# Performance work log

Measured on AMD Instinct MI355X. Metric: run time of the kernel, lower is better.

## Reference

```python
import jax, jax.numpy as jnp
import numpy as np

H = 8  # n_heads (init_kwarg, closed over)


def setup_inputs() -> dict:
    key = jax.random.key(0)
    ks = jax.random.split(key, 5)
    B, T, D, L = 8, 4096, 512, 128
    # lecun_normal: std = 1/sqrt(fan_in), fan_in = first dim here
    X = jax.random.normal(ks[0], (B, T, D), dtype=jnp.float32)
    Wk = jax.random.normal(ks[1], (D, L), dtype=jnp.float32) / np.sqrt(D)
    Wq = jax.random.normal(ks[2], (D, L), dtype=jnp.float32) / np.sqrt(D)
    Wv = jax.random.normal(ks[3], (D, D), dtype=jnp.float32) / np.sqrt(D)
    o_proj = jax.random.normal(ks[4], (D, D), dtype=jnp.float32) / np.sqrt(D)
    return {"X": X, "Wk": Wk, "Wq": Wq, "Wv": Wv, "o_proj": o_proj}


def reference(X, Wk, Wq, Wv, o_proj):
    B, T, D = X.shape
    L = Wk.shape[1]
    Dh, Lh = D // H, L // H
    # time-major projections: (T, B, H, *)
    V = jnp.einsum('DM,BTD->TBM', Wv, X).reshape(T, B, H, Dh)
    Q = jnp.einsum('DL,BTD->TBL', Wq, X).reshape(T, B, H, Lh)
    K = jnp.einsum('DL,BTD->TBL', Wk, X).reshape(T, B, H, Lh)
    scale = jax.lax.rsqrt(jnp.array(Dh, dtype=jnp.float32))
    K_exp = jnp.exp(K * scale)                      # (T,B,H,Lh)
    alpha = jnp.cumsum(K_exp, axis=0)               # causal normalizer
    Qs = jax.nn.softmax(Q * scale, axis=-1) / alpha # (T,B,H,Lh)

    def step(carry, args):
        qs_t, ke_t, v_t = args
        carry = carry + jnp.einsum('bhl,bhd->bhld', ke_t, v_t)
        y_t = jnp.einsum('bhl,bhld->bhd', qs_t, carry)
        return carry, y_t

    init = jnp.zeros((B, H, Lh, Dh), dtype=X.dtype)
    _, y = jax.lax.scan(step, init, (Qs, K_exp, V), unroll=16)  # y: (T,B,H,Dh)
    # faithful to source: transpose(3,0,1,2) then reshape(B,T,D)
    y = y.transpose(3, 0, 1, 2).reshape(B, T, D)
    return y @ o_proj
```

## Files before the change

### kernel.cpp

```cpp
#include <hip/hip_runtime.h>
#include <hip/hip_bf16.h>

#define B_ 8
#define T_ 4096
#define D_ 512
#define L_ 128
#define H_ 8
#define Dh_ 64
#define Lh_ 16
#define M_ (B_*T_)
#define SCALE 0.125f

typedef __bf16 v8bf __attribute__((ext_vector_type(8)));
typedef float  v4f  __attribute__((ext_vector_type(4)));
typedef unsigned short u16;
typedef u16 v8u __attribute__((ext_vector_type(8)));

__device__ __forceinline__ float b2f(u16 h){
    unsigned int u = ((unsigned int)h) << 16;
    return __builtin_bit_cast(float, u);
}
__device__ __forceinline__ u16 f2bf(float f){
    unsigned int u = __builtin_bit_cast(unsigned int, f);
    u += 0x7FFFu + ((u >> 16) & 1u);
    return (u16)(u >> 16);
}

__device__ __forceinline__ void wave_fence() {
    asm volatile("" ::: "memory");
}

__device__ __forceinline__ void gload16(const u16* g, u16* l) {
    __builtin_amdgcn_global_load_lds(
        (const __attribute__((address_space(1))) unsigned int*)(g),
        (__attribute__((address_space(3))) unsigned int*)(l), 16, 0, 0);
}

__global__ __launch_bounds__(256) void prep(
        const float* __restrict__ X,  const float* __restrict__ Wq,
        const float* __restrict__ Wk, const float* __restrict__ Wv,
        const float* __restrict__ Wo,
        u16* __restrict__ Xb, u16* __restrict__ WT, u16* __restrict__ OT)
{
    int bid = blockIdx.x;
    if (bid < 8192) {
        const size_t i = (size_t)bid * 256 + threadIdx.x;
        const float4* s = (const float4*)X + i * 2;
        float4 a = s[0], b = s[1];
        v8u o;
        o[0] = f2bf(a.x); o[1] = f2bf(a.y); o[2] = f2bf(a.z); o[3] = f2bf(a.w);
        o[4] = f2bf(b.x); o[5] = f2bf(b.y); o[6] = f2bf(b.z); o[7] = f2bf(b.w);
        *((v8u*)Xb + i) = o;
        return;
    }
    bid -= 8192;
    const float* src; u16* dst; int cols, bx, by;
    if (bid < 64)       { src = Wq; dst = WT;             cols = 128; bx = bid & 3;  by = bid >> 2; }
    else if (bid < 128) { src = Wk; dst = WT + 128 * 512; cols = 128; bid -= 64;  bx = bid & 3;  by = bid >> 2; }
    else if (bid < 384) { src = Wv; dst = WT + 256 * 512; cols = 512; bid -= 128; bx = bid & 15; by = bid >> 4; }
    else                { src = Wo; dst = OT;             cols = 512; bid -= 384; bx = bid & 15; by = bid >> 4; }
    __shared__ u16 tile[32][33];
    const int tx = threadIdx.x & 31, ty = threadIdx.x >> 5;
    const int c0 = bx * 32, r0 = by * 32;
    #pragma unroll
    for (int i = 0; i < 32; i += 8)
        tile[ty + i][tx] = f2bf(src[(size_t)(r0 + ty + i) * cols + c0 + tx]);
    __syncthreads();
    #pragma unroll
    for (int i = 0; i < 32; i += 8)
        dst[(size_t)(c0 + ty + i) * 512 + r0 + tx] = tile[tx][ty + i];
}

template<int MODE, int NY>
__global__ __launch_bounds__(256) void gemm_mfma(
        const u16* __restrict__ A, const u16* __restrict__ Bt,
        float* __restrict__ Qo, u16* __restrict__ KEo,
        u16* __restrict__ Vo, float* __restrict__ OutF)
{
    __shared__ __align__(16) u16 As[128 * 64];
    __shared__ __align__(16) u16 Bs[128 * 64];
    const int tid  = threadIdx.x;
    const int wave = tid >> 6, lane = tid & 63;
    const int wm = wave >> 1, wn = wave & 1;
    const int lm = lane & 15, quad = lane >> 4;

    const int bid = blockIdx.x;
    const int xcd = bid & 7, j = bid >> 3;
    const int grp = j / (8 * NY), r = j % (8 * NY);
    const int by  = r >> 3, pin = r & 7;
    const int bx  = xcd * 32 + grp * 8 + pin;
    const int gm0 = bx * 128, gn0 = by * 128;

    const int srow0 = wave * 32 + (lane >> 3);
    const int sg    = lane & 7;

    v4f acc[4][4];
    #pragma unroll
    for (int i = 0; i < 4; i++)
        #pragma unroll
        for (int j2 = 0; j2 < 4; j2++)
            acc[i][j2] = (v4f){0.f, 0.f, 0.f, 0.f};

    for (int kt = 0; kt < 8; ++kt) {
        const int k0 = kt * 64;
        #pragma unroll
        for (int rr = 0; rr < 4; ++rr) {
            const int row = srow0 + rr * 8;
            const int col = ((sg ^ (row & 7)) << 3) + k0;
            gload16(&A [(size_t)(gm0 + row) * 512 + col], &As[(wave * 4 + rr) * 512]);
            gload16(&Bt[(size_t)(gn0 + row) * 512 + col], &Bs[(wave * 4 + rr) * 512]);
        }
        __syncthreads();
        v8bf af[2][4], bfr[2][4];
        #pragma unroll
        for (int ks = 0; ks < 2; ks++)
            #pragma unroll
            for (int mi = 0; mi < 4; mi++) {
                const int g  = ks * 4 + quad;
                const int ra = wm * 64 + mi * 16 + lm;
                const int rb = wn * 64 + mi * 16 + lm;
                af [ks][mi] = *(const v8bf*)&As[ra * 64 + ((g ^ (ra & 7)) << 3)];
                bfr[ks][mi] = *(const v8bf*)&Bs[rb * 64 + ((g ^ (rb & 7)) << 3)];
            }
        #pragma unroll
        for (int ks = 0; ks < 2; ks++)
            #pragma unroll
            for (int mi = 0; mi < 4; mi++)
                #pragma unroll
                for (int ni = 0; ni < 4; ni++)
                    acc[mi][ni] = __builtin_amdgcn_mfma_f32_16x16x32_bf16(
                                      af[ks][mi], bfr[ks][ni], acc[mi][ni], 0, 0, 0);
        __syncthreads();
    }

    if (MODE == 1) {
        #pragma unroll
        for (int mi = 0; mi < 4; mi++)
          #pragma unroll
          for (int ni = 0; ni < 4; ni++)
            #pragma unroll
            for (int i = 0; i < 4; i++) {
                int row = gm0 + wm * 64 + mi * 16 + quad * 4 + i;
                int col = gn0 + wn * 64 + ni * 16 + lm;
                OutF[(size_t)row * 512 + col] = acc[mi][ni][i];
            }
    } else if (gn0 == 0) {
        #pragma unroll
        for (int mi = 0; mi < 4; mi++)
          #pragma unroll
          for (int ni = 0; ni < 4; ni++)
            #pragma unroll
            for (int i = 0; i < 4; i++) {
                int row = gm0 + wm * 64 + mi * 16 + quad * 4 + i;
                int col = wn * 64 + ni * 16 + lm;
                float qv = acc[mi][ni][i] * SCALE;
                float m = qv;
                #pragma unroll
                for (int off = 1; off < 16; off <<= 1) m = fmaxf(m, __shfl_xor(m, off));
                float e = __expf(qv - m);
                float s = e;
                #pragma unroll
                for (int off = 1; off < 16; off <<= 1) s += __shfl_xor(s, off);
                Qo[(size_t)row * 128 + col] = e / s;
            }
    } else if (gn0 == 128) {
        #pragma unroll
        for (int mi = 0; mi < 4; mi++)
          #pragma unroll
          for (int ni = 0; ni < 4; ni++)
            #pragma unroll
            for (int i = 0; i < 4; i++) {
                int row = gm0 + wm * 64 + mi * 16 + quad * 4 + i;
                int col = wn * 64 + ni * 16 + lm;
                KEo[(size_t)row * 128 + col] = f2bf(__expf(acc[mi][ni][i] * SCALE));
            }
    } else {
        #pragma unroll
        for (int mi = 0; mi < 4; mi++)
          #pragma unroll
          for (int ni = 0; ni < 4; ni++)
            #pragma unroll
            for (int i = 0; i < 4; i++) {
                int row = gm0 + wm * 64 + mi * 16 + quad * 4 + i;
                int col = gn0 + wn * 64 + ni * 16 + lm - 256;
                Vo[(size_t)row * 512 + col] = f2bf(acc[mi][ni][i]);
            }
    }
}

__global__ __launch_bounds__(256, 2) void chunk_sums_mfma(
        const u16* __restrict__ KE, const u16* __restrict__ V,
        float* __restrict__ Mc, float* __restrict__ AB)
{
    struct CLDS { u16 KA[16][72]; u16 VT[64][72]; };
    __shared__ __align__(16) CLDS lds[4];
    const int tid = threadIdx.x, wave = tid >> 6, lane = tid & 63;
    const int lm = lane & 15, quad = lane >> 4;
    const int ch = blockIdx.x * 4 + wave;
    const int bh = ch >> 6, c = ch & 63, b = bh >> 3, h = bh & 7;
    const int t0 = b * T_ + c * 64;
    CLDS& L = lds[wave];

    {
        const u16* kp = KE + (size_t)(t0 + lane) * L_ + h * Lh_;
        v8u k0 = *(const v8u*)kp, k1 = *(const v8u*)(kp + 8);
        #pragma unroll
        for (int l = 0; l < 8; l++) L.KA[l][lane]     = k0[l];
        #pragma unroll
        for (int l = 0; l < 8; l++) L.KA[l + 8][lane] = k1[l];
        const u16* vp = V + (size_t)(t0 + lane) * D_ + h * Dh_;
        #pragma unroll
        for (int seg = 0; seg < 8; ++seg) {
            v8u pv = *(const v8u*)(vp + seg * 8);
            #pragma unroll
            for (int j = 0; j < 8; j++) L.VT[seg * 8 + j][lane] = pv[j];
        }
    }
    wave_fence();

    v8bf ka[2];
    #pragma unroll
    for (int ki = 0; ki < 2; ki++)
        ka[ki] = *(const v8bf*)&L.KA[lm][ki * 32 + quad * 8];

    v8u onesu;
    #pragma unroll
    for (int j = 0; j < 8; j++) onesu[j] = 0x3F80;
    v8bf ones = __builtin_bit_cast(v8bf, onesu);

    v4f accL = (v4f){0.f, 0.f, 0.f, 0.f};
    accL = __builtin_amdgcn_mfma_f32_16x16x32_bf16(ka[0], ones, accL, 0, 0, 0);
    accL = __builtin_amdgcn_mfma_f32_16x16x32_bf16(ka[1], ones, accL, 0, 0, 0);

    v4f accM[4];
    #pragma unroll
    for (int nd = 0; nd < 4; nd++) accM[nd] = (v4f){0.f, 0.f, 0.f, 0.f};
    #pragma unroll
    for (int nd = 0; nd < 4; nd++)
        #pragma unroll
        for (int ki = 0; ki < 2; ki++) {
            v8bf vb = *(const v8bf*)&L.VT[nd * 16 + lm][ki * 32 + quad * 8];
            accM[nd] = __builtin_amdgcn_mfma_f32_16x16x32_bf16(ka[ki], vb, accM[nd], 0, 0, 0);
        }

    float* mcb = Mc + (size_t)ch * 1024;
    #pragma unroll
    for (int nd = 0; nd < 4; nd++)
        #pragma unroll
        for (int i = 0; i < 4; i++)
            mcb[(quad * 4 + i) * 64 + nd * 16 + lm] = accM[nd][i];
    if (lm == 0) {
        #pragma unroll
        for (int i = 0; i < 4; i++) AB[ch * 16 + quad * 4 + i] = accL[i];
    }
}

__global__ __launch_bounds__(256) void chunk_prefix(
        const float* __restrict__ Mc, u16* __restrict__ McB,
        float* __restrict__ AB)
{
    const int bh = blockIdx.x >> 2, qq = blockIdx.x & 3;
    const int i = qq * 256 + threadIdx.x;
    const size_t base = (size_t)bh * 64 * 1024 + i;
    float v[64];
    #pragma unroll
    for (int c = 0; c < 64; ++c) v[c] = Mc[base + (size_t)c * 1024];
    float run = 0.f;
    #pragma unroll
    for (int c = 0; c < 64; ++c) {
        McB[base + (size_t)c * 1024] = f2bf(run);
        run += v[c];
    }
    if (qq == 0 && threadIdx.x < 16) {
        const int l = threadIdx.x;
        float a[64];
        #pragma unroll
        for (int c = 0; c < 64; ++c) a[c] = AB[(bh * 64 + c) * 16 + l];
        float r2 = 0.f;
        #pragma unroll
        for (int c = 0; c < 64; ++c) {
            AB[(bh * 64 + c) * 16 + l] = r2;
            r2 += a[c];
        }
    }
}

__global__ __launch_bounds__(256, 2) void intra_mfma(
        const float* __restrict__ QS, const u16* __restrict__ KE,
        const u16* __restrict__ V, const u16* __restrict__ McB,
        const float* __restrict__ AB, u16* __restrict__ Y)
{
    struct ILDS {
        union {
            struct { u16 KA[16][72]; u16 Sc[16][72]; u16 qs[64][40]; } s;
            u16 p[64][72];
        } r;
        u16 VT[64][72];
    };
    __shared__ __align__(16) ILDS lds[4];
    const int tid = threadIdx.x, wave = tid >> 6, lane = tid & 63;
    const int lm = lane & 15, quad = lane >> 4;
    const int ch = blockIdx.x * 4 + wave;
    const int bh = ch >> 6, c = ch & 63, b = bh >> 3, h = bh & 7;
    const int t0 = b * T_ + c * 64;
    ILDS& L = lds[wave];

    {
        const u16* kp = KE + (size_t)(t0 + lane) * L_ + h * Lh_;
        v8u k0 = *(const v8u*)kp, k1 = *(const v8u*)(kp + 8);
        #pragma unroll
        for (int l = 0; l < 8; l++) L.r.s.KA[l][lane]     = k0[l];
        #pragma unroll
        for (int l = 0; l < 8; l++) L.r.s.KA[l + 8][lane] = k1[l];
        const u16* vp = V + (size_t)(t0 + lane) * D_ + h * Dh_;
        #pragma unroll
        for (int seg = 0; seg < 8; ++seg) {
            v8u pv = *(const v8u*)(vp + seg * 8);
            #pragma unroll
            for (int j = 0; j < 8; j++) L.VT[seg * 8 + j][lane] = pv[j];
        }
        const u16* mcb = McB + (size_t)ch * 1024;
        #pragma unroll
        for (int l = 0; l < 16; l++)
            L.r.s.Sc[l][lane] = mcb[l * 64 + lane];
        v8u z8;
        #pragma unroll
        for (int j = 0; j < 8; j++) z8[j] = 0;
        *(v8u*)&L.r.s.qs[lane][16] = z8;
        *(v8u*)&L.r.s.qs[lane][24] = z8;
    }
    const float ab = AB[ch * 16 + lm];
    wave_fence();

    v4f acc_a[4];
    #pragma unroll
    for (int mi = 0; mi < 4; mi++) acc_a[mi] = (v4f){ab, ab, ab, ab};
    #pragma unroll
    for (int mi = 0; mi < 4; mi++)
        #pragma unroll
        for (int ki = 0; ki < 2; ki++) {
            if (ki == 1 && mi < 2) continue;
            v8u ta;
            #pragma unroll
            for (int j = 0; j < 8; j++)
                ta[j] = (ki * 32 + quad * 8 + j <= mi * 16 + lm) ? (u16)0x3F80 : (u16)0;
            v8bf kb = *(const v8bf*)&L.r.s.KA[lm][ki * 32 + quad * 8];
            acc_a[mi] = __builtin_amdgcn_mfma_f32_16x16x32_bf16(
                            __builtin_bit_cast(v8bf, ta), kb, acc_a[mi], 0, 0, 0);
        }

    #pragma unroll
    for (int mi = 0; mi < 4; mi++)
        #pragma unroll
        for (int i = 0; i < 4; i++) {
            int t = mi * 16 + quad * 4 + i;
            float qs = QS[(size_t)(t0 + t) * L_ + h * Lh_ + lm];
            L.r.s.qs[t][lm] = f2bf(qs / acc_a[mi][i]);
        }
    wave_fence();

    v8bf aq[4];
    #pragma unroll
    for (int mi = 0; mi < 4; mi++)
        aq[mi] = *(const v8bf*)&L.r.s.qs[mi * 16 + lm][quad * 8];

    v4f accP[4][4], accY[4][4];
    #pragma unroll
    for (int mi = 0; mi < 4; mi++)
        #pragma unroll
        for (int ni = 0; ni < 4; ni++) {
            accP[mi][ni] = (v4f){0.f, 0.f, 0.f, 0.f};
            accY[mi][ni] = (v4f){0.f, 0.f, 0.f, 0.f};
        }

    #pragma unroll
    for (int ni = 0; ni < 4; ni++) {
        v8u kbu;
        #pragma unroll
        for (int j = 0; j < 8; j++) kbu[j] = 0;
        if (quad < 2) {
            #pragma unroll
            for (int j = 0; j < 8; j++)
                kbu[j] = L.r.s.KA[quad * 8 + j][ni * 16 + lm];
        }
        v8bf kbf = __builtin_bit_cast(v8bf, kbu);
        #pragma unroll
        for (int mi = ni; mi < 4; mi++)
            accP[mi][ni] = __builtin_amdgcn_mfma_f32_16x16x32_bf16(
                               aq[mi], kbf, accP[mi][ni], 0, 0, 0);
    }
    #pragma unroll
    for (int nd = 0; nd < 4; nd++) {
        v8u scu;
        #pragma unroll
        for (int j = 0; j < 8; j++) scu[j] = 0;
        if (quad < 2) {
            #pragma unroll
            for (int j = 0; j < 8; j++)
                scu[j] = L.r.s.Sc[quad * 8 + j][nd * 16 + lm];
        }
        v8bf scf = __builtin_bit_cast(v8bf, scu);
        #pragma unroll
        for (int mi = 0; mi < 4; mi++)
            accY[mi][nd] = __builtin_amdgcn_mfma_f32_16x16x32_bf16(
                               aq[mi], scf, accY[mi][nd], 0, 0, 0);
    }
    wave_fence();

    #pragma unroll
    for (int mi = 0; mi < 4; mi++)
        #pragma unroll
        for (int ni = 0; ni < 4; ni++)
            #pragma unroll
            for (int i = 0; i < 4; i++) {
                int t = mi * 16 + quad * 4 + i, tp = ni * 16 + lm;
                float pv = (ni < mi) ? accP[mi][ni][i]
                          : (ni == mi ? ((tp <= t) ? accP[mi][ni][i] : 0.f) : 0.f);
                L.r.p[t][tp] = f2bf(pv);
            }
    wave_fence();

    v8bf vb[4][2];
    #pragma unroll
    for (int nd = 0; nd < 4; nd++)
        #pragma unroll
        for (int ki = 0; ki < 2; ki++)
            vb[nd][ki] = *(const v8bf*)&L.VT[nd * 16 + lm][ki * 32 + quad * 8];
    #pragma unroll
    for (int mi = 0; mi < 4; mi++)
        #pragma unroll
        for (int ki = 0; ki < 2; ki++) {
            if (ki == 1 && mi < 2) continue;
            v8bf pa = *(const v8bf*)&L.r.p[mi * 16 + lm][ki * 32 + quad * 8];
            #pragma unroll
            for (int nd = 0; nd < 4; nd++)
                accY[mi][nd] = __builtin_amdgcn_mfma_f32_16x16x32_bf16(
                                   pa, vb[nd][ki], accY[mi][nd], 0, 0, 0);
        }

    #pragma unroll
    for (int mi = 0; mi < 4; mi++)
        #pragma unroll
        for (int nd = 0; nd < 4; nd++)
            #pragma unroll
            for (int i = 0; i < 4; i++) {
                int t = mi * 16 + quad * 4 + i;
                Y[(((size_t)(c * 64 + t)) * 64 + bh) * 64 + nd * 16 + lm] =
                    f2bf(accY[mi][nd][i]);
            }
}

__global__ __launch_bounds__(256) void transpose_Y(
        const u16* __restrict__ Y, u16* __restrict__ Z)
{
    __shared__ __align__(16) u16 tile[4][64][72];
    const int wave = threadIdx.x >> 6, t = threadIdx.x & 63;
    const int g = blockIdx.x * 4 + wave;
    u16 (*tl)[72] = tile[wave];
    const u16* yp = Y + (size_t)(g * 64 + t) * 64;
    #pragma unroll
    for (int seg = 0; seg < 8; ++seg)
        *(v8u*)&tl[t][seg * 8] = *(const v8u*)(yp + seg * 8);
    wave_fence();
    const int cl = t & 7, dq = t >> 3;
    #pragma unroll
    for (int p = 0; p < 8; ++p) {
        const int dh = p * 8 + dq;
        v8u pk;
        #pragma unroll
        for (int j = 0; j < 8; j++) pk[j] = tl[cl * 8 + j][dh];
        *(v8u*)&Z[(size_t)dh * 262144 + (size_t)g * 64 + cl * 8] = pk;
    }
}

extern "C" void kernel_launch(void* const* d_in, const int* in_sizes, int n_in,
                              void* d_out, int out_size, void* d_ws, size_t ws_size,
                              hipStream_t stream)
{
    (void)in_sizes; (void)n_in; (void)out_size; (void)ws_size;
    const float* X  = (const float*)d_in[0];
    const float* Wk = (const float*)d_in[1];
    const float* Wq = (const float*)d_in[2];
    const float* Wv = (const float*)d_in[3];
    const float* Wo = (const float*)d_in[4];
    float* Out = (float*)d_out;

    char* p = (char*)d_ws;
    auto alloc = [&](size_t bytes) { char* r = p; p += (bytes + 255) & ~(size_t)255; return r; };
    u16*   Xb = (u16*)  alloc((size_t)M_ * 512 * 2);
    u16*   WT = (u16*)  alloc((size_t)768 * 512 * 2);
    u16*   OT = (u16*)  alloc((size_t)512 * 512 * 2);
    u16*   V  = (u16*)  alloc((size_t)M_ * 512 * 2);
    float* Mc = (float*)alloc((size_t)4096 * 1024 * 4);
    float* AB = (float*)alloc((size_t)4096 * 16 * 4);
    float* Q  = (float*)alloc((size_t)M_ * 128 * 4);
    u16*   KE = (u16*)  alloc((size_t)M_ * 128 * 2);
    u16*   Y  = (u16*)  alloc((size_t)M_ * 512 * 2);
    u16*   Z  = (u16*)Mc;
    u16*   McB = (u16*)Xb;

    prep<<<8832, 256, 0, stream>>>(X, Wq, Wk, Wv, Wo, Xb, WT, OT);

    gemm_mfma<0, 6><<<1536, 256, 0, stream>>>(Xb, WT, Q, KE, V, nullptr);
    chunk_sums_mfma<<<1024, 256, 0, stream>>>(KE, V, Mc, AB);
    chunk_prefix   <<<256,  256, 0, stream>>>(Mc, McB, AB);
    intra_mfma     <<<1024, 256, 0, stream>>>(Q, KE, V, McB, AB, Y);
    transpose_Y    <<<1024, 256, 0, stream>>>(Y, Z);
    gemm_mfma<1, 4><<<1024, 256, 0, stream>>>(Z, OT, nullptr, nullptr, nullptr, Out);
}
```

Measured before the change: 248.5 us.

## Restructure GEMM into 256x256 double-buffered pipelined tiles with 512 threads

The bf16 MFMA GEMM moves from 128x128 tiles with 4 waves to 256x256 tiles with 8 waves. It double-buffers K-slices in LDS, using explicit vmcnt waits and barriers so the next global-to-LDS load overlaps the MFMAs, and raises wave priority around the MFMA block. The epilogue is remapped so one tile covers Q softmax and K exp together. The transpose_Y kernel now writes to LDS transposed and reads vectorised. The larger tiles improve operand reuse and hide load latency, but raise register pressure and leave fewer blocks (384/256) to fill the GPU.

```diff
diff --git a/kernel.cpp b/kernel.cpp
--- a/kernel.cpp
+++ b/kernel.cpp
@@ -35,6 +35,13 @@
         (const __attribute__((address_space(1))) unsigned int*)(g),
         (__attribute__((address_space(3))) unsigned int*)(l), 16, 0, 0);
 }
+
+#define PIPE_SYNC(N) do {                                        \
+    asm volatile("s_waitcnt vmcnt(" #N ")" ::: "memory");        \
+    __builtin_amdgcn_s_barrier();                                \
+    asm volatile("" ::: "memory");                               \
+    __builtin_amdgcn_sched_barrier(0);                           \
+} while (0)
 
 __global__ __launch_bounds__(256) void prep(
         const float* __restrict__ X,  const float* __restrict__ Wq,
@@ -72,116 +79,131 @@
 }
 
 template<int MODE, int NY>
-__global__ __launch_bounds__(256) void gemm_mfma(
+__global__ __launch_bounds__(512, 2) void gemm_mfma(
         const u16* __restrict__ A, const u16* __restrict__ Bt,
         float* __restrict__ Qo, u16* __restrict__ KEo,
         u16* __restrict__ Vo, float* __restrict__ OutF)
 {
-    __shared__ __align__(16) u16 As[128 * 64];
-    __shared__ __align__(16) u16 Bs[128 * 64];
+    __shared__ __align__(16) u16 lds[2][2][2][256 * 32];
     const int tid  = threadIdx.x;
     const int wave = tid >> 6, lane = tid & 63;
-    const int wm = wave >> 1, wn = wave & 1;
+    const int wm = wave >> 2, wn = wave & 3;
     const int lm = lane & 15, quad = lane >> 4;
 
     const int bid = blockIdx.x;
-    const int xcd = bid & 7, j = bid >> 3;
-    const int grp = j / (8 * NY), r = j % (8 * NY);
-    const int by  = r >> 3, pin = r & 7;
-    const int bx  = xcd * 32 + grp * 8 + pin;
-    const int gm0 = bx * 128, gn0 = by * 128;
-
-    const int srow0 = wave * 32 + (lane >> 3);
-    const int sg    = lane & 7;
-
-    v4f acc[4][4];
-    #pragma unroll
-    for (int i = 0; i < 4; i++)
-        #pragma unroll
-        for (int j2 = 0; j2 < 4; j2++)
-            acc[i][j2] = (v4f){0.f, 0.f, 0.f, 0.f};
-
-    for (int kt = 0; kt < 8; ++kt) {
-        const int k0 = kt * 64;
-        #pragma unroll
-        for (int rr = 0; rr < 4; ++rr) {
-            const int row = srow0 + rr * 8;
-            const int col = ((sg ^ (row & 7)) << 3) + k0;
-            gload16(&A [(size_t)(gm0 + row) * 512 + col], &As[(wave * 4 + rr) * 512]);
-            gload16(&Bt[(size_t)(gn0 + row) * 512 + col], &Bs[(wave * 4 + rr) * 512]);
-        }
-        __syncthreads();
-        v8bf af[2][4], bfr[2][4];
-        #pragma unroll
-        for (int ks = 0; ks < 2; ks++)
-            #pragma unroll
-            for (int mi = 0; mi < 4; mi++) {
-                const int g  = ks * 4 + quad;
-                const int ra = wm * 64 + mi * 16 + lm;
-                const int rb = wn * 64 + mi * 16 + lm;
-                af [ks][mi] = *(const v8bf*)&As[ra * 64 + ((g ^ (ra & 7)) << 3)];
-                bfr[ks][mi] = *(const v8bf*)&Bs[rb * 64 + ((g ^ (rb & 7)) << 3)];
-            }
-        #pragma unroll
-        for (int ks = 0; ks < 2; ks++)
-            #pragma unroll
-            for (int mi = 0; mi < 4; mi++)
-                #pragma unroll
-                for (int ni = 0; ni < 4; ni++)
-                    acc[mi][ni] = __builtin_amdgcn_mfma_f32_16x16x32_bf16(
-                                      af[ks][mi], bfr[ks][ni], acc[mi][ni], 0, 0, 0);
-        __syncthreads();
+    const int xcd = bid & 7, idx = bid >> 3;
+    const int by  = idx / 16, px = idx % 16;
+    const int bx  = xcd * 16 + px;
+    const int gm0 = bx * 256, gn0 = by * 256;
+
+    const int s0 = tid, s1 = tid + 512;
+
+    v4f acc[8][4];
+    #pragma unroll
+    for (int i = 0; i < 8; i++)
+        #pragma unroll
+        for (int j = 0; j < 4; j++)
+            acc[i][j] = (v4f){0.f, 0.f, 0.f, 0.f};
+
+    auto stageG = [&](int bsel, int ks, int kt) {
+        {
+            const u16* src = A + (size_t)gm0 * 512 + kt * 64 + ks * 32;
+            u16* dst = &lds[bsel][0][ks][wave * 512];
+            gload16(src + (size_t)(s0 >> 2) * 512 + (s0 & 3) * 8, dst);
+            gload16(src + (size_t)(s1 >> 2) * 512 + (s1 & 3) * 8, dst + 4096);
+        }
+        {
+            const u16* src = Bt + (size_t)gn0 * 512 + kt * 64 + ks * 32;
+            u16* dst = &lds[bsel][1][ks][wave * 512];
+            gload16(src + (size_t)(s0 >> 2) * 512 + (s0 & 3) * 8, dst);
+            gload16(src + (size_t)(s1 >> 2) * 512 + (s1 & 3) * 8, dst + 4096);
+        }
+    };
+
+    auto mma_phase = [&](int bsel, int ks) {
+        const u16* Ab = &lds[bsel][0][ks][0];
+        const u16* Bb = &lds[bsel][1][ks][0];
+        v8bf bfr[4], af[8];
+        #pragma unroll
+        for (int ni = 0; ni < 4; ni++)
+            bfr[ni] = *(const v8bf*)&Bb[(wn * 64 + ni * 16 + lm) * 32 + quad * 8];
+        #pragma unroll
+        for (int mi = 0; mi < 8; mi++)
+            af[mi] = *(const v8bf*)&Ab[(wm * 128 + mi * 16 + lm) * 32 + quad * 8];
+        __builtin_amdgcn_s_setprio(1);
+        #pragma unroll
+        for (int mi = 0; mi < 8; mi++)
+            #pragma unroll
+            for (int ni = 0; ni < 4; ni++)
+                acc[mi][ni] = __builtin_amdgcn_mfma_f32_16x16x32_bf16(
+                                  af[mi], bfr[ni], acc[mi][ni], 0, 0, 0);
+        __builtin_amdgcn_s_setprio(0);
+    };
+
+    stageG(0, 0, 0);
+    stageG(0, 1, 0);
+
+    for (int t = 0; t < 8; ++t) {
+        const int cur = t & 1;
+        if (t < 7) { stageG(cur ^ 1, 0, t + 1); PIPE_SYNC(8); }
+        else       {                            PIPE_SYNC(4); }
+        mma_phase(cur, 0);
+        if (t < 7) { stageG(cur ^ 1, 1, t + 1); PIPE_SYNC(8); }
+        else       {                            PIPE_SYNC(0); }
+        mma_phase(cur, 1);
     }
 
     if (MODE == 1) {
         #pragma unroll
-        for (int mi = 0; mi < 4; mi++)
+        for (int mi = 0; mi < 8; mi++)
           #pragma unroll
           for (int ni = 0; ni < 4; ni++)
             #pragma unroll
             for (int i = 0; i < 4; i++) {
-                int row = gm0 + wm * 64 + mi * 16 + quad * 4 + i;
+                int row = gm0 + wm * 128 + mi * 16 + quad * 4 + i;
                 int col = gn0 + wn * 64 + ni * 16 + lm;
                 OutF[(size_t)row * 512 + col] = acc[mi][ni][i];
             }
     } else if (gn0 == 0) {
-        #pragma unroll
-        for (int mi = 0; mi < 4; mi++)
+        if (wn < 2) {
+            #pragma unroll
+            for (int mi = 0; mi < 8; mi++)
+              #pragma unroll
+              for (int ni = 0; ni < 4; ni++)
+                #pragma unroll
+                for (int i = 0; i < 4; i++) {
+                    int row = gm0 + wm * 128 + mi * 16 + quad * 4 + i;
+                    int col = wn * 64 + ni * 16 + lm;
+                    float qv = acc[mi][ni][i] * SCALE;
+                    float m = qv;
+                    #pragma unroll
+                    for (int off = 1; off < 16; off <<= 1) m = fmaxf(m, __shfl_xor(m, off));
+                    float e = __expf(qv - m);
+                    float s = e;
+                    #pragma unroll
+                    for (int off = 1; off < 16; off <<= 1) s += __shfl_xor(s, off);
+                    Qo[(size_t)row * 128 + col] = e / s;
+                }
+        } else {
+            #pragma unroll
+            for (int mi = 0; mi < 8; mi++)
+              #pragma unroll
+              for (int ni = 0; ni < 4; ni++)
+                #pragma unroll
+                for (int i = 0; i < 4; i++) {
+                    int row = gm0 + wm * 128 + mi * 16 + quad * 4 + i;
+                    int col = (wn - 2) * 64 + ni * 16 + lm;
+                    KEo[(size_t)row * 128 + col] = f2bf(__expf(acc[mi][ni][i] * SCALE));
+                }
+        }
+    } else {
+        #pragma unroll
+        for (int mi = 0; mi < 8; mi++)
           #pragma unroll
           for (int ni = 0; ni < 4; ni++)
             #pragma unroll
             for (int i = 0; i < 4; i++) {
-                int row = gm0 + wm * 64 + mi * 16 + quad * 4 + i;
-                int col = wn * 64 + ni * 16 + lm;
-                float qv = acc[mi][ni][i] * SCALE;
-                float m = qv;
-                #pragma unroll
-                for (int off = 1; off < 16; off <<= 1) m = fmaxf(m, __shfl_xor(m, off));
-                float e = __expf(qv - m);
-                float s = e;
-                #pragma unroll
-                for (int off = 1; off < 16; off <<= 1) s += __shfl_xor(s, off);
-                Qo[(size_t)row * 128 + col] = e / s;
-            }
-    } else if (gn0 == 128) {
-        #pragma unroll
-        for (int mi = 0; mi < 4; mi++)
-          #pragma unroll
-          for (int ni = 0; ni < 4; ni++)
-            #pragma unroll
-            for (int i = 0; i < 4; i++) {
-                int row = gm0 + wm * 64 + mi * 16 + quad * 4 + i;
-                int col = wn * 64 + ni * 16 + lm;
-                KEo[(size_t)row * 128 + col] = f2bf(__expf(acc[mi][ni][i] * SCALE));
-            }
-    } else {
-        #pragma unroll
-        for (int mi = 0; mi < 4; mi++)
-          #pragma unroll
-          for (int ni = 0; ni < 4; ni++)
-            #pragma unroll
-            for (int i = 0; i < 4; i++) {
-                int row = gm0 + wm * 64 + mi * 16 + quad * 4 + i;
+                int row = gm0 + wm * 128 + mi * 16 + quad * 4 + i;
                 int col = gn0 + wn * 64 + ni * 16 + lm - 256;
                 Vo[(size_t)row * 512 + col] = f2bf(acc[mi][ni][i]);
             }
@@ -459,16 +481,17 @@
     u16 (*tl)[72] = tile[wave];
     const u16* yp = Y + (size_t)(g * 64 + t) * 64;
     #pragma unroll
-    for (int seg = 0; seg < 8; ++seg)
-        *(v8u*)&tl[t][seg * 8] = *(const v8u*)(yp + seg * 8);
+    for (int seg = 0; seg < 8; ++seg) {
+        v8u v = *(const v8u*)(yp + seg * 8);
+        #pragma unroll
+        for (int j = 0; j < 8; j++) tl[seg * 8 + j][t] = v[j];
+    }
     wave_fence();
     const int cl = t & 7, dq = t >> 3;
     #pragma unroll
     for (int p = 0; p < 8; ++p) {
         const int dh = p * 8 + dq;
-        v8u pk;
-        #pragma unroll
-        for (int j = 0; j < 8; j++) pk[j] = tl[cl * 8 + j][dh];
+        v8u pk = *(const v8u*)&tl[dh][cl * 8];
         *(v8u*)&Z[(size_t)dh * 262144 + (size_t)g * 64 + cl * 8] = pk;
     }
 }
@@ -501,10 +524,10 @@
 
     prep<<<8832, 256, 0, stream>>>(X, Wq, Wk, Wv, Wo, Xb, WT, OT);
 
-    gemm_mfma<0, 6><<<1536, 256, 0, stream>>>(Xb, WT, Q, KE, V, nullptr);
+    gemm_mfma<0, 3><<<384, 512, 0, stream>>>(Xb, WT, Q, KE, V, nullptr);
     chunk_sums_mfma<<<1024, 256, 0, stream>>>(KE, V, Mc, AB);
     chunk_prefix   <<<256,  256, 0, stream>>>(Mc, McB, AB);
     intra_mfma     <<<1024, 256, 0, stream>>>(Q, KE, V, McB, AB, Y);
     transpose_Y    <<<1024, 256, 0, stream>>>(Y, Z);
-    gemm_mfma<1, 4><<<1024, 256, 0, stream>>>(Z, OT, nullptr, nullptr, nullptr, Out);
-}
+    gemm_mfma<1, 2><<<256, 512, 0, stream>>>(Z, OT, nullptr, nullptr, nullptr, Out);
+}
```

Measured after the change: 253.4 us. No clear change (+2.0%).

## Store V pre-transposed per chunk and load operands via async global-to-LDS

Applied to the files above, without the earlier changes.

The projection GEMM epilogue now transposes V tiles through shared memory and writes them in a per-(batch,head,chunk) d-major layout. The chunk-sum and intra-chunk kernels can then pull V, KE and the prefix state straight into LDS with swizzled global_load_lds, replacing scalar scatter-transposes. The prefix kernel writes the state pre-transposed, and transpose_Y moves its scatter to the write side. The cost is an extra LDS pass and barrier in the GEMM epilogue, plus explicit vmcnt drains.

```diff
diff --git a/kernel.cpp b/kernel.cpp
--- a/kernel.cpp
+++ b/kernel.cpp
@@ -29,6 +29,11 @@
 __device__ __forceinline__ void wave_fence() {
     asm volatile("" ::: "memory");
 }
+
+#define DRAIN_GLDS() do {                                        \
+    asm volatile("s_waitcnt vmcnt(0)" ::: "memory");             \
+    __builtin_amdgcn_sched_barrier(0);                           \
+} while (0)
 
 __device__ __forceinline__ void gload16(const u16* g, u16* l) {
     __builtin_amdgcn_global_load_lds(
@@ -75,10 +80,12 @@
 __global__ __launch_bounds__(256) void gemm_mfma(
         const u16* __restrict__ A, const u16* __restrict__ Bt,
         float* __restrict__ Qo, u16* __restrict__ KEo,
-        u16* __restrict__ Vo, float* __restrict__ OutF)
-{
-    __shared__ __align__(16) u16 As[128 * 64];
-    __shared__ __align__(16) u16 Bs[128 * 64];
+        u16* __restrict__ VTo, float* __restrict__ OutF)
+{
+    __shared__ __align__(16) union GS {
+        struct { u16 As[128 * 64]; u16 Bs[128 * 64]; } s;
+        u16 vt[128][136];
+    } smem;
     const int tid  = threadIdx.x;
     const int wave = tid >> 6, lane = tid & 63;
     const int wm = wave >> 1, wn = wave & 1;
@@ -107,8 +114,8 @@
         for (int rr = 0; rr < 4; ++rr) {
             const int row = srow0 + rr * 8;
             const int col = ((sg ^ (row & 7)) << 3) + k0;
-            gload16(&A [(size_t)(gm0 + row) * 512 + col], &As[(wave * 4 + rr) * 512]);
-            gload16(&Bt[(size_t)(gn0 + row) * 512 + col], &Bs[(wave * 4 + rr) * 512]);
+            gload16(&A [(size_t)(gm0 + row) * 512 + col], &smem.s.As[(wave * 4 + rr) * 512]);
+            gload16(&Bt[(size_t)(gn0 + row) * 512 + col], &smem.s.Bs[(wave * 4 + rr) * 512]);
         }
         __syncthreads();
         v8bf af[2][4], bfr[2][4];
@@ -119,8 +126,8 @@
                 const int g  = ks * 4 + quad;
                 const int ra = wm * 64 + mi * 16 + lm;
                 const int rb = wn * 64 + mi * 16 + lm;
-                af [ks][mi] = *(const v8bf*)&As[ra * 64 + ((g ^ (ra & 7)) << 3)];
-                bfr[ks][mi] = *(const v8bf*)&Bs[rb * 64 + ((g ^ (rb & 7)) << 3)];
+                af [ks][mi] = *(const v8bf*)&smem.s.As[ra * 64 + ((g ^ (ra & 7)) << 3)];
+                bfr[ks][mi] = *(const v8bf*)&smem.s.Bs[rb * 64 + ((g ^ (rb & 7)) << 3)];
             }
         #pragma unroll
         for (int ks = 0; ks < 2; ks++)
@@ -181,18 +188,28 @@
           for (int ni = 0; ni < 4; ni++)
             #pragma unroll
             for (int i = 0; i < 4; i++) {
-                int row = gm0 + wm * 64 + mi * 16 + quad * 4 + i;
-                int col = gn0 + wn * 64 + ni * 16 + lm - 256;
-                Vo[(size_t)row * 512 + col] = f2bf(acc[mi][ni][i]);
-            }
+                int cloc = wn * 64 + ni * 16 + lm;
+                int tloc = wm * 64 + mi * 16 + quad * 4 + i;
+                smem.vt[cloc][tloc] = f2bf(acc[mi][ni][i]);
+            }
+        __syncthreads();
+        const int b   = gm0 >> 12, tau0 = gm0 & 4095, c0 = tau0 >> 6;
+        const int h0  = (gn0 - 256) >> 6;
+        const int d   = tid & 63, cl_ = (tid >> 6) & 1, hl = tid >> 7;
+        const int bh  = b * 8 + h0 + hl;
+        u16* dst = VTo + (((size_t)bh * 64 + (c0 + cl_)) * 64 + d) * 64;
+        const u16* srow = &smem.vt[hl * 64 + d][cl_ * 64];
+        #pragma unroll
+        for (int k = 0; k < 8; ++k)
+            *(v8u*)(dst + k * 8) = *(const v8u*)(srow + k * 8);
     }
 }
 
 __global__ __launch_bounds__(256, 2) void chunk_sums_mfma(
-        const u16* __restrict__ KE, const u16* __restrict__ V,
+        const u16* __restrict__ KE, const u16* __restrict__ VTg,
         float* __restrict__ Mc, float* __restrict__ AB)
 {
-    struct CLDS { u16 KA[16][72]; u16 VT[64][72]; };
+    struct CLDS { u16 KA[16][72]; u16 VT[64][64]; };
     __shared__ __align__(16) CLDS lds[4];
     const int tid = threadIdx.x, wave = tid >> 6, lane = tid & 63;
     const int lm = lane & 15, quad = lane >> 4;
@@ -202,19 +219,19 @@
     CLDS& L = lds[wave];
 
     {
+        const u16* vsrc = VTg + ((size_t)bh * 64 + c) * 4096;
+        #pragma unroll
+        for (int k = 0; k < 8; ++k) {
+            const int d = k * 8 + (lane >> 3);
+            const int g = (lane & 7) ^ (lane >> 3);
+            gload16(vsrc + d * 64 + g * 8, &L.VT[k * 8][0]);
+        }
         const u16* kp = KE + (size_t)(t0 + lane) * L_ + h * Lh_;
         v8u k0 = *(const v8u*)kp, k1 = *(const v8u*)(kp + 8);
         #pragma unroll
         for (int l = 0; l < 8; l++) L.KA[l][lane]     = k0[l];
         #pragma unroll
         for (int l = 0; l < 8; l++) L.KA[l + 8][lane] = k1[l];
-        const u16* vp = V + (size_t)(t0 + lane) * D_ + h * Dh_;
-        #pragma unroll
-        for (int seg = 0; seg < 8; ++seg) {
-            v8u pv = *(const v8u*)(vp + seg * 8);
-            #pragma unroll
-            for (int j = 0; j < 8; j++) L.VT[seg * 8 + j][lane] = pv[j];
-        }
     }
     wave_fence();
 
@@ -232,6 +249,8 @@
     accL = __builtin_amdgcn_mfma_f32_16x16x32_bf16(ka[0], ones, accL, 0, 0, 0);
     accL = __builtin_amdgcn_mfma_f32_16x16x32_bf16(ka[1], ones, accL, 0, 0, 0);
 
+    DRAIN_GLDS();
+
     v4f accM[4];
     #pragma unroll
     for (int nd = 0; nd < 4; nd++) accM[nd] = (v4f){0.f, 0.f, 0.f, 0.f};
@@ -239,7 +258,8 @@
     for (int nd = 0; nd < 4; nd++)
         #pragma unroll
         for (int ki = 0; ki < 2; ki++) {
-            v8bf vb = *(const v8bf*)&L.VT[nd * 16 + lm][ki * 32 + quad * 8];
+            const int row = nd * 16 + lm;
+            v8bf vb = *(const v8bf*)&L.VT[row][(((ki * 4 + quad) ^ (lm & 7)) << 3)];
             accM[nd] = __builtin_amdgcn_mfma_f32_16x16x32_bf16(ka[ki], vb, accM[nd], 0, 0, 0);
         }
 
@@ -260,15 +280,16 @@
         float* __restrict__ AB)
 {
     const int bh = blockIdx.x >> 2, qq = blockIdx.x & 3;
-    const int i = qq * 256 + threadIdx.x;
-    const size_t base = (size_t)bh * 64 * 1024 + i;
+    const int j = qq * 256 + threadIdx.x;
+    const int iin = ((j & 15) << 6) + (j >> 4);
+    const size_t bbase = (size_t)bh * 65536;
     float v[64];
     #pragma unroll
-    for (int c = 0; c < 64; ++c) v[c] = Mc[base + (size_t)c * 1024];
+    for (int c = 0; c < 64; ++c) v[c] = Mc[bbase + (size_t)c * 1024 + iin];
     float run = 0.f;
     #pragma unroll
     for (int c = 0; c < 64; ++c) {
-        McB[base + (size_t)c * 1024] = f2bf(run);
+        McB[bbase + (size_t)c * 1024 + j] = f2bf(run);
         run += v[c];
     }
     if (qq == 0 && threadIdx.x < 16) {
@@ -287,15 +308,15 @@
 
 __global__ __launch_bounds__(256, 2) void intra_mfma(
         const float* __restrict__ QS, const u16* __restrict__ KE,
-        const u16* __restrict__ V, const u16* __restrict__ McB,
+        const u16* __restrict__ VTg, const u16* __restrict__ McB,
         const float* __restrict__ AB, u16* __restrict__ Y)
 {
     struct ILDS {
         union {
-            struct { u16 KA[16][72]; u16 Sc[16][72]; u16 qs[64][40]; } s;
+            struct { u16 KA[16][72]; u16 KEO[64][16]; u16 ScT[64][16]; u16 qs[64][40]; } s;
             u16 p[64][72];
         } r;
-        u16 VT[64][72];
+        u16 VT[64][64];
     };
     __shared__ __align__(16) ILDS lds[4];
     const int tid = threadIdx.x, wave = tid >> 6, lane = tid & 63;
@@ -306,23 +327,26 @@
     ILDS& L = lds[wave];
 
     {
+        const u16* vsrc = VTg + ((size_t)bh * 64 + c) * 4096;
+        #pragma unroll
+        for (int k = 0; k < 8; ++k) {
+            const int d = k * 8 + (lane >> 3);
+            const int g = (lane & 7) ^ (lane >> 3);
+            gload16(vsrc + d * 64 + g * 8, &L.VT[k * 8][0]);
+        }
+        #pragma unroll
+        for (int k = 0; k < 2; ++k) {
+            const int slot = k * 64 + lane;
+            gload16(KE + (size_t)(t0 + (slot >> 1)) * L_ + h * Lh_ + (slot & 1) * 8,
+                    &L.r.s.KEO[k * 32][0]);
+            gload16(McB + (size_t)ch * 1024 + slot * 8, &L.r.s.ScT[k * 32][0]);
+        }
         const u16* kp = KE + (size_t)(t0 + lane) * L_ + h * Lh_;
         v8u k0 = *(const v8u*)kp, k1 = *(const v8u*)(kp + 8);
         #pragma unroll
         for (int l = 0; l < 8; l++) L.r.s.KA[l][lane]     = k0[l];
         #pragma unroll
         for (int l = 0; l < 8; l++) L.r.s.KA[l + 8][lane] = k1[l];
-        const u16* vp = V + (size_t)(t0 + lane) * D_ + h * Dh_;
-        #pragma unroll
-        for (int seg = 0; seg < 8; ++seg) {
-            v8u pv = *(const v8u*)(vp + seg * 8);
-            #pragma unroll
-            for (int j = 0; j < 8; j++) L.VT[seg * 8 + j][lane] = pv[j];
-        }
-        const u16* mcb = McB + (size_t)ch * 1024;
-        #pragma unroll
-        for (int l = 0; l < 16; l++)
-            L.r.s.Sc[l][lane] = mcb[l * 64 + lane];
         v8u z8;
         #pragma unroll
         for (int j = 0; j < 8; j++) z8[j] = 0;
@@ -364,6 +388,8 @@
     for (int mi = 0; mi < 4; mi++)
         aq[mi] = *(const v8bf*)&L.r.s.qs[mi * 16 + lm][quad * 8];
 
+    DRAIN_GLDS();
+
     v4f accP[4][4], accY[4][4];
     #pragma unroll
     for (int mi = 0; mi < 4; mi++)
@@ -373,17 +399,15 @@
             accY[mi][ni] = (v4f){0.f, 0.f, 0.f, 0.f};
         }
 
+    v8u zero8;
+    #pragma unroll
+    for (int j = 0; j < 8; j++) zero8[j] = 0;
+
     #pragma unroll
     for (int ni = 0; ni < 4; ni++) {
-        v8u kbu;
-        #pragma unroll
-        for (int j = 0; j < 8; j++) kbu[j] = 0;
-        if (quad < 2) {
-            #pragma unroll
-            for (int j = 0; j < 8; j++)
-                kbu[j] = L.r.s.KA[quad * 8 + j][ni * 16 + lm];
-        }
-        v8bf kbf = __builtin_bit_cast(v8bf, kbu);
+        v8bf kbf = (quad < 2)
+            ? *(const v8bf*)&L.r.s.KEO[ni * 16 + lm][quad * 8]
+            : __builtin_bit_cast(v8bf, zero8);
         #pragma unroll
         for (int mi = ni; mi < 4; mi++)
             accP[mi][ni] = __builtin_amdgcn_mfma_f32_16x16x32_bf16(
@@ -391,15 +415,9 @@
     }
     #pragma unroll
     for (int nd = 0; nd < 4; nd++) {
-        v8u scu;
-        #pragma unroll
-        for (int j = 0; j < 8; j++) scu[j] = 0;
-        if (quad < 2) {
-            #pragma unroll
-            for (int j = 0; j < 8; j++)
-                scu[j] = L.r.s.Sc[quad * 8 + j][nd * 16 + lm];
-        }
-        v8bf scf = __builtin_bit_cast(v8bf, scu);
+        v8bf scf = (quad < 2)
+            ? *(const v8bf*)&L.r.s.ScT[nd * 16 + lm][quad * 8]
+            : __builtin_bit_cast(v8bf, zero8);
         #pragma unroll
         for (int mi = 0; mi < 4; mi++)
             accY[mi][nd] = __builtin_amdgcn_mfma_f32_16x16x32_bf16(
@@ -420,12 +438,6 @@
             }
     wave_fence();
 
-    v8bf vb[4][2];
-    #pragma unroll
-    for (int nd = 0; nd < 4; nd++)
-        #pragma unroll
-        for (int ki = 0; ki < 2; ki++)
-            vb[nd][ki] = *(const v8bf*)&L.VT[nd * 16 + lm][ki * 32 + quad * 8];
     #pragma unroll
     for (int mi = 0; mi < 4; mi++)
         #pragma unroll
@@ -433,9 +445,12 @@
             if (ki == 1 && mi < 2) continue;
             v8bf pa = *(const v8bf*)&L.r.p[mi * 16 + lm][ki * 32 + quad * 8];
             #pragma unroll
-            for (int nd = 0; nd < 4; nd++)
+            for (int nd = 0; nd < 4; nd++) {
+                const int row = nd * 16 + lm;
+                v8bf vb = *(const v8bf*)&L.VT[row][(((ki * 4 + quad) ^ (lm & 7)) << 3)];
                 accY[mi][nd] = __builtin_amdgcn_mfma_f32_16x16x32_bf16(
-                                   pa, vb[nd][ki], accY[mi][nd], 0, 0, 0);
+                                   pa, vb, accY[mi][nd], 0, 0, 0);
+            }
         }
 
     #pragma unroll
@@ -459,16 +474,17 @@
     u16 (*tl)[72] = tile[wave];
     const u16* yp = Y + (size_t)(g * 64 + t) * 64;
     #pragma unroll
-    for (int seg = 0; seg < 8; ++seg)
-        *(v8u*)&tl[t][seg * 8] = *(const v8u*)(yp + seg * 8);
+    for (int seg = 0; seg < 8; ++seg) {
+        v8u v = *(const v8u*)(yp + seg * 8);
+        #pragma unroll
+        for (int j = 0; j < 8; j++) tl[seg * 8 + j][t] = v[j];
+    }
     wave_fence();
     const int cl = t & 7, dq = t >> 3;
     #pragma unroll
     for (int p = 0; p < 8; ++p) {
         const int dh = p * 8 + dq;
-        v8u pk;
-        #pragma unroll
-        for (int j = 0; j < 8; j++) pk[j] = tl[cl * 8 + j][dh];
+        v8u pk = *(const v8u*)&tl[dh][cl * 8];
         *(v8u*)&Z[(size_t)dh * 262144 + (size_t)g * 64 + cl * 8] = pk;
     }
 }
@@ -487,24 +503,24 @@
 
     char* p = (char*)d_ws;
     auto alloc = [&](size_t bytes) { char* r = p; p += (bytes + 255) & ~(size_t)255; return r; };
-    u16*   Xb = (u16*)  alloc((size_t)M_ * 512 * 2);
-    u16*   WT = (u16*)  alloc((size_t)768 * 512 * 2);
-    u16*   OT = (u16*)  alloc((size_t)512 * 512 * 2);
-    u16*   V  = (u16*)  alloc((size_t)M_ * 512 * 2);
-    float* Mc = (float*)alloc((size_t)4096 * 1024 * 4);
-    float* AB = (float*)alloc((size_t)4096 * 16 * 4);
-    float* Q  = (float*)alloc((size_t)M_ * 128 * 4);
-    u16*   KE = (u16*)  alloc((size_t)M_ * 128 * 2);
-    u16*   Y  = (u16*)  alloc((size_t)M_ * 512 * 2);
-    u16*   Z  = (u16*)Mc;
+    u16*   Xb  = (u16*)  alloc((size_t)M_ * 512 * 2);
+    u16*   WT  = (u16*)  alloc((size_t)768 * 512 * 2);
+    u16*   OT  = (u16*)  alloc((size_t)512 * 512 * 2);
+    u16*   VTg = (u16*)  alloc((size_t)M_ * 512 * 2);
+    float* Mc  = (float*)alloc((size_t)4096 * 1024 * 4);
+    float* AB  = (float*)alloc((size_t)4096 * 16 * 4);
+    float* Q   = (float*)alloc((size_t)M_ * 128 * 4);
+    u16*   KE  = (u16*)  alloc((size_t)M_ * 128 * 2);
+    u16*   Y   = (u16*)  alloc((size_t)M_ * 512 * 2);
+    u16*   Z   = (u16*)Mc;
     u16*   McB = (u16*)Xb;
 
     prep<<<8832, 256, 0, stream>>>(X, Wq, Wk, Wv, Wo, Xb, WT, OT);
 
-    gemm_mfma<0, 6><<<1536, 256, 0, stream>>>(Xb, WT, Q, KE, V, nullptr);
-    chunk_sums_mfma<<<1024, 256, 0, stream>>>(KE, V, Mc, AB);
+    gemm_mfma<0, 6><<<1536, 256, 0, stream>>>(Xb, WT, Q, KE, VTg, nullptr);
+    chunk_sums_mfma<<<1024, 256, 0, stream>>>(KE, VTg, Mc, AB);
     chunk_prefix   <<<256,  256, 0, stream>>>(Mc, McB, AB);
-    intra_mfma     <<<1024, 256, 0, stream>>>(Q, KE, V, McB, AB, Y);
+    intra_mfma     <<<1024, 256, 0, stream>>>(Q, KE, VTg, McB, AB, Y);
     transpose_Y    <<<1024, 256, 0, stream>>>(Y, Z);
     gemm_mfma<1, 4><<<1024, 256, 0, stream>>>(Z, OT, nullptr, nullptr, nullptr, Out);
 }
```

Measured after the change: 258.8 us. +4.2%, slower.

## Halve GEMM K-tile to 32 and transpose Y tile on write side

Applied to the files above, without the earlier changes.

The MFMA GEMM now steps through K in 32-wide slices over 16 iterations instead of 64-wide over 8. This halves LDS use per block, which may allow more resident blocks, but doubles the number of barriers and load phases, and it uses a new 4-way XOR swizzle. Separately, transpose_Y now scatters elements into LDS already transposed, so the read side becomes a single 16-byte vector load instead of eight strided scalar reads. The intent is to trade strided LDS reads for strided LDS writes.

```diff
diff --git a/kernel.cpp b/kernel.cpp
--- a/kernel.cpp
+++ b/kernel.cpp
@@ -77,8 +77,8 @@
         float* __restrict__ Qo, u16* __restrict__ KEo,
         u16* __restrict__ Vo, float* __restrict__ OutF)
 {
-    __shared__ __align__(16) u16 As[128 * 64];
-    __shared__ __align__(16) u16 Bs[128 * 64];
+    __shared__ __align__(16) u16 As[128 * 32];
+    __shared__ __align__(16) u16 Bs[128 * 32];
     const int tid  = threadIdx.x;
     const int wave = tid >> 6, lane = tid & 63;
     const int wm = wave >> 1, wn = wave & 1;
@@ -91,8 +91,8 @@
     const int bx  = xcd * 32 + grp * 8 + pin;
     const int gm0 = bx * 128, gn0 = by * 128;
 
-    const int srow0 = wave * 32 + (lane >> 3);
-    const int sg    = lane & 7;
+    const int row0 = tid >> 2,  pos0 = tid & 3;
+    const int pos1 = pos0;
 
     v4f acc[4][4];
     #pragma unroll
@@ -101,35 +101,32 @@
         for (int j2 = 0; j2 < 4; j2++)
             acc[i][j2] = (v4f){0.f, 0.f, 0.f, 0.f};
 
-    for (int kt = 0; kt < 8; ++kt) {
-        const int k0 = kt * 64;
-        #pragma unroll
-        for (int rr = 0; rr < 4; ++rr) {
-            const int row = srow0 + rr * 8;
-            const int col = ((sg ^ (row & 7)) << 3) + k0;
-            gload16(&A [(size_t)(gm0 + row) * 512 + col], &As[(wave * 4 + rr) * 512]);
-            gload16(&Bt[(size_t)(gn0 + row) * 512 + col], &Bs[(wave * 4 + rr) * 512]);
+    for (int kt = 0; kt < 16; ++kt) {
+        const int k0 = kt * 32;
+        {
+            const int c0a = ((pos0 ^ (row0 & 3)) << 3) + k0;
+            const int r1  = row0 + 64;
+            const int c1a = ((pos1 ^ (r1 & 3)) << 3) + k0;
+            gload16(&A [(size_t)(gm0 + row0) * 512 + c0a], &As[wave * 512]);
+            gload16(&A [(size_t)(gm0 + r1  ) * 512 + c1a], &As[wave * 512 + 2048]);
+            gload16(&Bt[(size_t)(gn0 + row0) * 512 + c0a], &Bs[wave * 512]);
+            gload16(&Bt[(size_t)(gn0 + r1  ) * 512 + c1a], &Bs[wave * 512 + 2048]);
         }
         __syncthreads();
-        v8bf af[2][4], bfr[2][4];
-        #pragma unroll
-        for (int ks = 0; ks < 2; ks++)
-            #pragma unroll
-            for (int mi = 0; mi < 4; mi++) {
-                const int g  = ks * 4 + quad;
-                const int ra = wm * 64 + mi * 16 + lm;
-                const int rb = wn * 64 + mi * 16 + lm;
-                af [ks][mi] = *(const v8bf*)&As[ra * 64 + ((g ^ (ra & 7)) << 3)];
-                bfr[ks][mi] = *(const v8bf*)&Bs[rb * 64 + ((g ^ (rb & 7)) << 3)];
-            }
-        #pragma unroll
-        for (int ks = 0; ks < 2; ks++)
-            #pragma unroll
-            for (int mi = 0; mi < 4; mi++)
-                #pragma unroll
-                for (int ni = 0; ni < 4; ni++)
-                    acc[mi][ni] = __builtin_amdgcn_mfma_f32_16x16x32_bf16(
-                                      af[ks][mi], bfr[ks][ni], acc[mi][ni], 0, 0, 0);
+        v8bf af[4], bfr[4];
+        #pragma unroll
+        for (int mi = 0; mi < 4; mi++) {
+            const int ra = wm * 64 + mi * 16 + lm;
+            const int rb = wn * 64 + mi * 16 + lm;
+            af [mi] = *(const v8bf*)&As[ra * 32 + ((quad ^ (ra & 3)) << 3)];
+            bfr[mi] = *(const v8bf*)&Bs[rb * 32 + ((quad ^ (rb & 3)) << 3)];
+        }
+        #pragma unroll
+        for (int mi = 0; mi < 4; mi++)
+            #pragma unroll
+            for (int ni = 0; ni < 4; ni++)
+                acc[mi][ni] = __builtin_amdgcn_mfma_f32_16x16x32_bf16(
+                                  af[mi], bfr[ni], acc[mi][ni], 0, 0, 0);
         __syncthreads();
     }
 
@@ -459,16 +456,17 @@
     u16 (*tl)[72] = tile[wave];
     const u16* yp = Y + (size_t)(g * 64 + t) * 64;
     #pragma unroll
-    for (int seg = 0; seg < 8; ++seg)
-        *(v8u*)&tl[t][seg * 8] = *(const v8u*)(yp + seg * 8);
+    for (int seg = 0; seg < 8; ++seg) {
+        v8u v = *(const v8u*)(yp + seg * 8);
+        #pragma unroll
+        for (int j = 0; j < 8; j++) tl[seg * 8 + j][t] = v[j];
+    }
     wave_fence();
     const int cl = t & 7, dq = t >> 3;
     #pragma unroll
     for (int p = 0; p < 8; ++p) {
         const int dh = p * 8 + dq;
-        v8u pk;
-        #pragma unroll
-        for (int j = 0; j < 8; j++) pk[j] = tl[cl * 8 + j][dh];
+        v8u pk = *(const v8u*)&tl[dh][cl * 8];
         *(v8u*)&Z[(size_t)dh * 262144 + (size_t)g * 64 + cl * 8] = pk;
     }
 }
```

Result: slower. 261.6 us (+5.3%).
